# Kernel tuning notes

Measured on AMD Instinct MI355X. Metric: run time of the kernel, lower is better.

The kernel has to match this reference:

```python
import jax, jax.numpy as jnp
import numpy as np

# Gate hyperparameters (from init_kwargs)
DIM = 4096
N_EXPERTS = 256        # n_routed_experts
N_GROUPS = 8           # n_expert_groups
TOPK_GROUPS = 4        # n_limited_groups
TOPK = 8               # n_activated_experts
ROUTE_SCALE = 1.0
N_TOKENS = 16384       # batch * seq_len flattened


def setup_inputs() -> dict:
    key = jax.random.key(0)
    kx, kw = jax.random.split(key)
    x = jax.random.normal(kx, (N_TOKENS, DIM), dtype=jnp.float32)
    # xavier-ish scale for the gate projection weight [n_experts, dim]
    weight = jax.random.normal(kw, (N_EXPERTS, DIM), dtype=jnp.float32) * (1.0 / np.sqrt(DIM))
    return {"x": x, "weight": weight}


def reference(x, weight):
    T = x.shape[0]
    # scores = linear(x, weight)  -> [T, E]
    logits = jnp.einsum('td,ed->te', x, weight)
    # score_func == 'softmax' computed in fp32 (torch: softmax(dim=-1, dtype=float32))
    scores = jax.nn.softmax(logits.astype(jnp.float32), axis=-1)
    original_scores = scores

    # group-limited routing (n_groups > 1, no bias -> amax per group)
    sg = scores.reshape(T, N_GROUPS, N_EXPERTS // N_GROUPS)   # [T, G, E/G]
    group_scores = jnp.max(sg, axis=-1)                        # [T, G]
    _, gidx = jax.lax.top_k(group_scores, TOPK_GROUPS)         # [T, topk_groups]
    keep = jnp.zeros((T, N_GROUPS), dtype=bool)
    keep = keep.at[jnp.arange(T)[:, None], gidx].set(True)
    masked = jnp.where(keep[:, :, None], sg, -jnp.inf).reshape(T, N_EXPERTS)

    # top-k expert selection; weights gathered from the un-masked scores
    _, idx = jax.lax.top_k(masked, TOPK)                       # [T, topk]
    weights = jnp.take_along_axis(original_scores, idx, axis=1)
    weights = weights * ROUTE_SCALE
    return weights.astype(x.dtype), idx
```

## Files before the change

### kernel.cpp

```cpp
#include <hip/hip_runtime.h>
#include <math.h>
#include <stdint.h>

#define NTOK   16384
#define DIM    4096
#define NEXP   256
#define TOPKG  4
#define TOPK   8
#define NSPLIT 4
#define KCHUNK (DIM / NSPLIT)
#define BM     256
#define BK     32
#define NSTEPS (KCHUNK / BK)

typedef float v4f   __attribute__((ext_vector_type(4)));
typedef short short8 __attribute__((ext_vector_type(8)));

__device__ inline unsigned short f2bf(float x) {
    unsigned u = __float_as_uint(x);
    return (unsigned short)((u + 0x7fffu + ((u >> 16) & 1u)) >> 16);
}
__device__ inline float bf2f(unsigned short h) {
    return __uint_as_float(((unsigned)h) << 16);
}
__device__ inline int swz4(int row, int slot) { return slot ^ ((row >> 1) & 3); }

__global__ __launch_bounds__(256) void wprep(const float* __restrict__ W,
                                             unsigned short* __restrict__ Wh,
                                             unsigned short* __restrict__ Wl) {
    int i = (blockIdx.x * 256 + threadIdx.x) * 4;
    float4 v = *(const float4*)(W + i);
    ushort4 h, l;
    h.x = f2bf(v.x); l.x = f2bf(v.x - bf2f(h.x));
    h.y = f2bf(v.y); l.y = f2bf(v.y - bf2f(h.y));
    h.z = f2bf(v.z); l.z = f2bf(v.z - bf2f(h.z));
    h.w = f2bf(v.w); l.w = f2bf(v.w - bf2f(h.w));
    *(ushort4*)(Wh + i) = h;
    *(ushort4*)(Wl + i) = l;
}

__global__ __launch_bounds__(512, 2) void gate_gemm(const float* __restrict__ X,
                                                    const unsigned short* __restrict__ Wh,
                                                    const unsigned short* __restrict__ Wl,
                                                    float* __restrict__ P) {
    __shared__ __align__(16) unsigned short Ah[2][BM * BK];
    __shared__ __align__(16) unsigned short Al[2][BM * BK];
    __shared__ __align__(16) unsigned short Bh[2][NEXP * BK];
    __shared__ __align__(16) unsigned short Bl[2][NEXP * BK];

    const int t  = threadIdx.x;
    const int bm = blockIdx.x * BM;
    const int z  = blockIdx.y;
    const int k0 = z * KCHUNK;

    const int l  = t & 63;
    const int w  = t >> 6;
    const int wr = w >> 2;
    const int wc = w & 3;
    const int lm = l & 15;
    const int lq = l >> 4;

    const int ar = t >> 1;
    const float* xrow = X + (size_t)(bm + ar) * DIM + k0 + (t & 1) * 16;

    v4f acc[8][4] = {};

    {
#pragma unroll
        for (int i = 0; i < 2; ++i) {
            int flat = i * 512 + t;
            int e = flat >> 2, qq = flat & 3;
            const unsigned short* gh = Wh + (size_t)e * DIM + k0 + swz4(e, qq) * 8;
            const unsigned short* gl = Wl + (size_t)e * DIM + k0 + swz4(e, qq) * 8;
            __builtin_amdgcn_global_load_lds(
                (const __attribute__((address_space(1))) unsigned int*)gh,
                (__attribute__((address_space(3))) unsigned int*)&Bh[0][flat * 8], 16, 0, 0);
            __builtin_amdgcn_global_load_lds(
                (const __attribute__((address_space(1))) unsigned int*)gl,
                (__attribute__((address_space(3))) unsigned int*)&Bl[0][flat * 8], 16, 0, 0);
        }
        float4 xv0[4];
#pragma unroll
        for (int i = 0; i < 4; ++i) xv0[i] = *(const float4*)(xrow + i * 4);
#pragma unroll
        for (int i = 0; i < 4; ++i) {
            ushort4 h, lo;
            h.x = f2bf(xv0[i].x); lo.x = f2bf(xv0[i].x - bf2f(h.x));
            h.y = f2bf(xv0[i].y); lo.y = f2bf(xv0[i].y - bf2f(h.y));
            h.z = f2bf(xv0[i].z); lo.z = f2bf(xv0[i].z - bf2f(h.z));
            h.w = f2bf(xv0[i].w); lo.w = f2bf(xv0[i].w - bf2f(h.w));
            int j = (t & 1) * 4 + i;
            int idx = ar * BK + swz4(ar, j >> 1) * 8 + (j & 1) * 4;
            *(ushort4*)&Ah[0][idx] = h;
            *(ushort4*)&Al[0][idx] = lo;
        }
        __syncthreads();
    }

    int cur = 0;
    for (int s = 0; s < NSTEPS; ++s) {
        const int nxt = cur ^ 1;
        const bool pf = (s + 1 < NSTEPS);
        const int krn = (pf ? s + 1 : s) * BK;

        short8 bh[4], bl[4];
        float4 xv[4];

#pragma unroll
        for (int q = 0; q < 4; ++q) {
            if (q == 0) {
#pragma unroll
                for (int c = 0; c < 4; ++c) {
                    int e = wc * 64 + c * 16 + lm;
                    bh[c] = *(const short8*)&Bh[cur][e * BK + swz4(e, lq) * 8];
                    bl[c] = *(const short8*)&Bl[cur][e * BK + swz4(e, lq) * 8];
                }
            }
            const int m0 = wr * 128 + (2 * q) * 16 + lm;
            const int m1 = m0 + 16;
            short8 a0h = *(const short8*)&Ah[cur][m0 * BK + swz4(m0, lq) * 8];
            short8 a0l = *(const short8*)&Al[cur][m0 * BK + swz4(m0, lq) * 8];
            short8 a1h = *(const short8*)&Ah[cur][m1 * BK + swz4(m1, lq) * 8];
            short8 a1l = *(const short8*)&Al[cur][m1 * BK + swz4(m1, lq) * 8];

            if (pf) {
                if (q == 0) {
#pragma unroll
                    for (int i = 0; i < 4; ++i) xv[i] = *(const float4*)(xrow + krn + i * 4);
#pragma unroll
                    for (int i = 0; i < 2; ++i) {
                        int flat = i * 512 + t;
                        int e = flat >> 2, qq = flat & 3;
                        const unsigned short* g = Wh + (size_t)e * DIM + k0 + krn + swz4(e, qq) * 8;
                        __builtin_amdgcn_global_load_lds(
                            (const __attribute__((address_space(1))) unsigned int*)g,
                            (__attribute__((address_space(3))) unsigned int*)&Bh[nxt][flat * 8], 16, 0, 0);
                    }
                } else if (q == 1) {
#pragma unroll
                    for (int i = 0; i < 2; ++i) {
                        int flat = i * 512 + t;
                        int e = flat >> 2, qq = flat & 3;
                        const unsigned short* g = Wl + (size_t)e * DIM + k0 + krn + swz4(e, qq) * 8;
                        __builtin_amdgcn_global_load_lds(
                            (const __attribute__((address_space(1))) unsigned int*)g,
                            (__attribute__((address_space(3))) unsigned int*)&Bl[nxt][flat * 8], 16, 0, 0);
                    }
                } else {
                    const int i0 = (q == 2) ? 0 : 2;
#pragma unroll
                    for (int i = i0; i < i0 + 2; ++i) {
                        ushort4 h, lo;
                        h.x = f2bf(xv[i].x); lo.x = f2bf(xv[i].x - bf2f(h.x));
                        h.y = f2bf(xv[i].y); lo.y = f2bf(xv[i].y - bf2f(h.y));
                        h.z = f2bf(xv[i].z); lo.z = f2bf(xv[i].z - bf2f(h.z));
                        h.w = f2bf(xv[i].w); lo.w = f2bf(xv[i].w - bf2f(h.w));
                        int j = (t & 1) * 4 + i;
                        int idx = ar * BK + swz4(ar, j >> 1) * 8 + (j & 1) * 4;
                        *(ushort4*)&Ah[nxt][idx] = h;
                        *(ushort4*)&Al[nxt][idx] = lo;
                    }
                }
            }

            if (q == 0) asm volatile("s_waitcnt lgkmcnt(8)");
            __builtin_amdgcn_s_barrier();
            asm volatile("s_waitcnt lgkmcnt(0)");
            __builtin_amdgcn_sched_barrier(0);
            __builtin_amdgcn_s_setprio(1);
#pragma unroll
            for (int c = 0; c < 4; ++c) {
                acc[2 * q][c] = __builtin_amdgcn_mfma_f32_16x16x32_bf16(a0h, bh[c], acc[2 * q][c], 0, 0, 0);
                acc[2 * q][c] = __builtin_amdgcn_mfma_f32_16x16x32_bf16(a0h, bl[c], acc[2 * q][c], 0, 0, 0);
                acc[2 * q][c] = __builtin_amdgcn_mfma_f32_16x16x32_bf16(a0l, bh[c], acc[2 * q][c], 0, 0, 0);
            }
#pragma unroll
            for (int c = 0; c < 4; ++c) {
                acc[2 * q + 1][c] = __builtin_amdgcn_mfma_f32_16x16x32_bf16(a1h, bh[c], acc[2 * q + 1][c], 0, 0, 0);
                acc[2 * q + 1][c] = __builtin_amdgcn_mfma_f32_16x16x32_bf16(a1h, bl[c], acc[2 * q + 1][c], 0, 0, 0);
                acc[2 * q + 1][c] = __builtin_amdgcn_mfma_f32_16x16x32_bf16(a1l, bh[c], acc[2 * q + 1][c], 0, 0, 0);
            }
            __builtin_amdgcn_s_setprio(0);
            if (q < 3) __builtin_amdgcn_s_barrier();
            else       __syncthreads();
        }
        cur = nxt;
    }

    float* Pb = P + ((size_t)z * NTOK + bm) * NEXP;
#pragma unroll
    for (int r = 0; r < 8; ++r)
#pragma unroll
        for (int c = 0; c < 4; ++c)
#pragma unroll
            for (int g = 0; g < 4; ++g)
                Pb[(size_t)(wr * 128 + r * 16 + lq * 4 + g) * NEXP + wc * 64 + c * 16 + lm] = acc[r][c][g];
}

__global__ __launch_bounds__(256) void gate_route(const float* __restrict__ P,
                                                  float* __restrict__ outw,
                                                  float* __restrict__ outi) {
    const int lane = threadIdx.x & 63;
    const int tok  = (blockIdx.x * blockDim.x + threadIdx.x) >> 6;
    if (tok >= NTOK) return;

    float l[4] = {0.f, 0.f, 0.f, 0.f};
#pragma unroll
    for (int z = 0; z < NSPLIT; ++z) {
        float4 v = *(const float4*)(P + ((size_t)z * NTOK + tok) * NEXP + lane * 4);
        l[0] += v.x; l[1] += v.y; l[2] += v.z; l[3] += v.w;
    }

    float lmax = fmaxf(fmaxf(l[0], l[1]), fmaxf(l[2], l[3]));
    float m = lmax;
#pragma unroll
    for (int o = 32; o; o >>= 1) m = fmaxf(m, __shfl_xor(m, o));

    float s = __expf(l[0] - m) + __expf(l[1] - m) + __expf(l[2] - m) + __expf(l[3] - m);
#pragma unroll
    for (int o = 32; o; o >>= 1) s += __shfl_xor(s, o);

    float gm = lmax;
#pragma unroll
    for (int o = 4; o; o >>= 1) gm = fmaxf(gm, __shfl_xor(gm, o));

    const int g = lane >> 3;
    int rank = 0;
#pragma unroll
    for (int gg = 0; gg < 8; ++gg) {
        float vg = __shfl(gm, gg * 8);
        rank += (vg > gm) || (vg == gm && gg < g);
    }
    const bool allowed = rank < TOPKG;

    float mv[4];
#pragma unroll
    for (int j = 0; j < 4; ++j) mv[j] = allowed ? l[j] : -INFINITY;

    float wsel = 0.0f;
    int   isel = 0;

    for (int k = 0; k < TOPK; ++k) {
        float bv = mv[0];
        int   bi = lane * 4;
        if (mv[1] > bv) { bv = mv[1]; bi = lane * 4 + 1; }
        if (mv[2] > bv) { bv = mv[2]; bi = lane * 4 + 2; }
        if (mv[3] > bv) { bv = mv[3]; bi = lane * 4 + 3; }
#pragma unroll
        for (int o = 32; o; o >>= 1) {
            float ov = __shfl_xor(bv, o);
            int   oi = __shfl_xor(bi, o);
            if (ov > bv || (ov == bv && oi < bi)) { bv = ov; bi = oi; }
        }
        if (lane == k) { wsel = __expf(bv - m) / s; isel = bi; }
        if ((bi >> 2) == lane) mv[bi & 3] = -INFINITY;
    }

    if (lane < TOPK) {
        outw[(size_t)tok * TOPK + lane] = wsel;
        outi[(size_t)tok * TOPK + lane] = (float)isel;
    }
}

extern "C" void kernel_launch(void* const* d_in, const int* in_sizes, int n_in,
                              void* d_out, int out_size, void* d_ws, size_t ws_size,
                              hipStream_t stream) {
    const float* x  = (const float*)d_in[0];
    const float* wt = (const float*)d_in[1];

    float* P = (float*)d_ws;
    unsigned short* Wh = (unsigned short*)((char*)d_ws + (size_t)NSPLIT * NTOK * NEXP * 4);
    unsigned short* Wl = Wh + (size_t)NEXP * DIM;

    float* outw = (float*)d_out;
    float* outi = (float*)d_out + (size_t)NTOK * TOPK;

    wprep<<<(NEXP * DIM) / (256 * 4), 256, 0, stream>>>(wt, Wh, Wl);

    dim3 ggrid(NTOK / BM, NSPLIT);
    gate_gemm<<<ggrid, 512, 0, stream>>>(x, Wh, Wl, P);

    gate_route<<<(NTOK * 64) / 256, 256, 0, stream>>>(P, outw, outi);
}
```

Measured before the change: 438.6 us.

## Prepack weight hi/lo tiles contiguously and simplify GEMM pipeline to one barrier per step

The weight prep kernel now writes the bf16 hi/lo split into a pre-swizzled, per-K-step contiguous layout, so each GEMM step copies one contiguous block into LDS. The inner loop drops the four-phase interleaved barrier schedule and uses a single prefetch, compute, convert, sync sequence per K step. The 1D grid is remapped so that blocks sharing a K-split are grouped together, and the partial-result stores become nontemporal. This cuts address math and barriers, but removes the fine-grained overlap of X conversion with MFMA work.

```diff
diff --git a/kernel.cpp b/kernel.cpp
--- a/kernel.cpp
+++ b/kernel.cpp
@@ -26,32 +26,39 @@
 __device__ inline int swz4(int row, int slot) { return slot ^ ((row >> 1) & 3); }
 
 __global__ __launch_bounds__(256) void wprep(const float* __restrict__ W,
-                                             unsigned short* __restrict__ Wh,
-                                             unsigned short* __restrict__ Wl) {
-    int i = (blockIdx.x * 256 + threadIdx.x) * 4;
-    float4 v = *(const float4*)(W + i);
-    ushort4 h, l;
-    h.x = f2bf(v.x); l.x = f2bf(v.x - bf2f(h.x));
-    h.y = f2bf(v.y); l.y = f2bf(v.y - bf2f(h.y));
-    h.z = f2bf(v.z); l.z = f2bf(v.z - bf2f(h.z));
-    h.w = f2bf(v.w); l.w = f2bf(v.w - bf2f(h.w));
-    *(ushort4*)(Wh + i) = h;
-    *(ushort4*)(Wl + i) = l;
+                                             unsigned short* __restrict__ Wp) {
+    int u  = blockIdx.x * 256 + threadIdx.x;
+    int zs = u >> 11;
+    int c  = u & 2047;
+    int z  = zs >> 5, s = zs & 31;
+    int half = c >> 10;
+    int cc = c & 1023;
+    int e  = cc >> 2, sl = cc & 3;
+    int sig = swz4(e, sl);
+    const float* src = W + (size_t)e * DIM + z * KCHUNK + s * BK + sig * 8;
+    float4 v0 = *(const float4*)src;
+    float4 v1 = *(const float4*)(src + 4);
+    float xf[8] = {v0.x, v0.y, v0.z, v0.w, v1.x, v1.y, v1.z, v1.w};
+    short8 out;
+#pragma unroll
+    for (int j = 0; j < 8; ++j) {
+        unsigned short h = f2bf(xf[j]);
+        out[j] = half ? (short)f2bf(xf[j] - bf2f(h)) : (short)h;
+    }
+    *(short8*)(Wp + (size_t)u * 8) = out;
 }
 
 __global__ __launch_bounds__(512, 2) void gate_gemm(const float* __restrict__ X,
-                                                    const unsigned short* __restrict__ Wh,
-                                                    const unsigned short* __restrict__ Wl,
+                                                    const unsigned short* __restrict__ Wp,
                                                     float* __restrict__ P) {
+    __shared__ __align__(16) unsigned short Bbuf[2][NEXP * BK * 2];
     __shared__ __align__(16) unsigned short Ah[2][BM * BK];
     __shared__ __align__(16) unsigned short Al[2][BM * BK];
-    __shared__ __align__(16) unsigned short Bh[2][NEXP * BK];
-    __shared__ __align__(16) unsigned short Bl[2][NEXP * BK];
-
-    const int t  = threadIdx.x;
-    const int bm = blockIdx.x * BM;
-    const int z  = blockIdx.y;
-    const int k0 = z * KCHUNK;
+
+    const int t = threadIdx.x;
+    const int b  = blockIdx.x;
+    const int z  = (b & 7) >> 1;
+    const int bm = (2 * (b >> 3) + (b & 1)) * BM;
 
     const int l  = t & 63;
     const int w  = t >> 6;
@@ -60,28 +67,24 @@
     const int lm = l & 15;
     const int lq = l >> 4;
 
+    const unsigned short* wz = Wp + (size_t)z * NSTEPS * (NEXP * BK * 2);
+
     const int ar = t >> 1;
-    const float* xrow = X + (size_t)(bm + ar) * DIM + k0 + (t & 1) * 16;
+    const float* xrow = X + (size_t)(bm + ar) * DIM + z * KCHUNK + (t & 1) * 16;
 
     v4f acc[8][4] = {};
 
     {
-#pragma unroll
-        for (int i = 0; i < 2; ++i) {
-            int flat = i * 512 + t;
-            int e = flat >> 2, qq = flat & 3;
-            const unsigned short* gh = Wh + (size_t)e * DIM + k0 + swz4(e, qq) * 8;
-            const unsigned short* gl = Wl + (size_t)e * DIM + k0 + swz4(e, qq) * 8;
+        float4 xv0[4];
+#pragma unroll
+        for (int i = 0; i < 4; ++i) xv0[i] = *(const float4*)(xrow + i * 4);
+#pragma unroll
+        for (int j = 0; j < 4; ++j) {
+            int flat = j * 512 + t;
             __builtin_amdgcn_global_load_lds(
-                (const __attribute__((address_space(1))) unsigned int*)gh,
-                (__attribute__((address_space(3))) unsigned int*)&Bh[0][flat * 8], 16, 0, 0);
-            __builtin_amdgcn_global_load_lds(
-                (const __attribute__((address_space(1))) unsigned int*)gl,
-                (__attribute__((address_space(3))) unsigned int*)&Bl[0][flat * 8], 16, 0, 0);
-        }
-        float4 xv0[4];
-#pragma unroll
-        for (int i = 0; i < 4; ++i) xv0[i] = *(const float4*)(xrow + i * 4);
+                (const __attribute__((address_space(1))) unsigned int*)(wz + flat * 8),
+                (__attribute__((address_space(3))) unsigned int*)&Bbuf[0][flat * 8], 16, 0, 0);
+        }
 #pragma unroll
         for (int i = 0; i < 4; ++i) {
             ushort4 h, lo;
@@ -101,89 +104,61 @@
     for (int s = 0; s < NSTEPS; ++s) {
         const int nxt = cur ^ 1;
         const bool pf = (s + 1 < NSTEPS);
-        const int krn = (pf ? s + 1 : s) * BK;
+
+        float4 xv[4];
+        if (pf) {
+#pragma unroll
+            for (int i = 0; i < 4; ++i) xv[i] = *(const float4*)(xrow + (s + 1) * BK + i * 4);
+            const unsigned short* wsrc = wz + (size_t)(s + 1) * (NEXP * BK * 2);
+#pragma unroll
+            for (int j = 0; j < 4; ++j) {
+                int flat = j * 512 + t;
+                __builtin_amdgcn_global_load_lds(
+                    (const __attribute__((address_space(1))) unsigned int*)(wsrc + flat * 8),
+                    (__attribute__((address_space(3))) unsigned int*)&Bbuf[nxt][flat * 8], 16, 0, 0);
+            }
+        }
+        __builtin_amdgcn_sched_barrier(0);
 
         short8 bh[4], bl[4];
-        float4 xv[4];
-
-#pragma unroll
-        for (int q = 0; q < 4; ++q) {
-            if (q == 0) {
-#pragma unroll
-                for (int c = 0; c < 4; ++c) {
-                    int e = wc * 64 + c * 16 + lm;
-                    bh[c] = *(const short8*)&Bh[cur][e * BK + swz4(e, lq) * 8];
-                    bl[c] = *(const short8*)&Bl[cur][e * BK + swz4(e, lq) * 8];
-                }
+#pragma unroll
+        for (int c = 0; c < 4; ++c) {
+            int e = wc * 64 + c * 16 + lm;
+            bh[c] = *(const short8*)&Bbuf[cur][e * BK + swz4(e, lq) * 8];
+            bl[c] = *(const short8*)&Bbuf[cur][NEXP * BK + e * BK + swz4(e, lq) * 8];
+        }
+        __builtin_amdgcn_s_setprio(1);
+#pragma unroll
+        for (int r = 0; r < 8; ++r) {
+            int m = wr * 128 + r * 16 + lm;
+            short8 ah = *(const short8*)&Ah[cur][m * BK + swz4(m, lq) * 8];
+            short8 al = *(const short8*)&Al[cur][m * BK + swz4(m, lq) * 8];
+#pragma unroll
+            for (int c = 0; c < 4; ++c) {
+                acc[r][c] = __builtin_amdgcn_mfma_f32_16x16x32_bf16(ah, bh[c], acc[r][c], 0, 0, 0);
+                acc[r][c] = __builtin_amdgcn_mfma_f32_16x16x32_bf16(ah, bl[c], acc[r][c], 0, 0, 0);
+                acc[r][c] = __builtin_amdgcn_mfma_f32_16x16x32_bf16(al, bh[c], acc[r][c], 0, 0, 0);
             }
-            const int m0 = wr * 128 + (2 * q) * 16 + lm;
-            const int m1 = m0 + 16;
-            short8 a0h = *(const short8*)&Ah[cur][m0 * BK + swz4(m0, lq) * 8];
-            short8 a0l = *(const short8*)&Al[cur][m0 * BK + swz4(m0, lq) * 8];
-            short8 a1h = *(const short8*)&Ah[cur][m1 * BK + swz4(m1, lq) * 8];
-            short8 a1l = *(const short8*)&Al[cur][m1 * BK + swz4(m1, lq) * 8];
-
-            if (pf) {
-                if (q == 0) {
-#pragma unroll
-                    for (int i = 0; i < 4; ++i) xv[i] = *(const float4*)(xrow + krn + i * 4);
-#pragma unroll
-                    for (int i = 0; i < 2; ++i) {
-                        int flat = i * 512 + t;
-                        int e = flat >> 2, qq = flat & 3;
-                        const unsigned short* g = Wh + (size_t)e * DIM + k0 + krn + swz4(e, qq) * 8;
-                        __builtin_amdgcn_global_load_lds(
-                            (const __attribute__((address_space(1))) unsigned int*)g,
-                            (__attribute__((address_space(3))) unsigned int*)&Bh[nxt][flat * 8], 16, 0, 0);
-                    }
-                } else if (q == 1) {
-#pragma unroll
-                    for (int i = 0; i < 2; ++i) {
-                        int flat = i * 512 + t;
-                        int e = flat >> 2, qq = flat & 3;
-                        const unsigned short* g = Wl + (size_t)e * DIM + k0 + krn + swz4(e, qq) * 8;
-                        __builtin_amdgcn_global_load_lds(
-                            (const __attribute__((address_space(1))) unsigned int*)g,
-                            (__attribute__((address_space(3))) unsigned int*)&Bl[nxt][flat * 8], 16, 0, 0);
-                    }
-                } else {
-                    const int i0 = (q == 2) ? 0 : 2;
-#pragma unroll
-                    for (int i = i0; i < i0 + 2; ++i) {
-                        ushort4 h, lo;
-                        h.x = f2bf(xv[i].x); lo.x = f2bf(xv[i].x - bf2f(h.x));
-                        h.y = f2bf(xv[i].y); lo.y = f2bf(xv[i].y - bf2f(h.y));
-                        h.z = f2bf(xv[i].z); lo.z = f2bf(xv[i].z - bf2f(h.z));
-                        h.w = f2bf(xv[i].w); lo.w = f2bf(xv[i].w - bf2f(h.w));
-                        int j = (t & 1) * 4 + i;
-                        int idx = ar * BK + swz4(ar, j >> 1) * 8 + (j & 1) * 4;
-                        *(ushort4*)&Ah[nxt][idx] = h;
-                        *(ushort4*)&Al[nxt][idx] = lo;
-                    }
-                }
+        }
+        __builtin_amdgcn_s_setprio(0);
+        __builtin_amdgcn_sched_barrier(0);
+
+        if (pf) {
+#pragma unroll
+            for (int i = 0; i < 4; ++i) {
+                ushort4 h, lo;
+                h.x = f2bf(xv[i].x); lo.x = f2bf(xv[i].x - bf2f(h.x));
+                h.y = f2bf(xv[i].y); lo.y = f2bf(xv[i].y - bf2f(h.y));
+                h.z = f2bf(xv[i].z); lo.z = f2bf(xv[i].z - bf2f(h.z));
+                h.w = f2bf(xv[i].w); lo.w = f2bf(xv[i].w - bf2f(h.w));
+                int j = (t & 1) * 4 + i;
+                int idx = ar * BK + swz4(ar, j >> 1) * 8 + (j & 1) * 4;
+                *(ushort4*)&Ah[nxt][idx] = h;
+                *(ushort4*)&Al[nxt][idx] = lo;
             }
-
-            if (q == 0) asm volatile("s_waitcnt lgkmcnt(8)");
-            __builtin_amdgcn_s_barrier();
-            asm volatile("s_waitcnt lgkmcnt(0)");
-            __builtin_amdgcn_sched_barrier(0);
-            __builtin_amdgcn_s_setprio(1);
-#pragma unroll
-            for (int c = 0; c < 4; ++c) {
-                acc[2 * q][c] = __builtin_amdgcn_mfma_f32_16x16x32_bf16(a0h, bh[c], acc[2 * q][c], 0, 0, 0);
-                acc[2 * q][c] = __builtin_amdgcn_mfma_f32_16x16x32_bf16(a0h, bl[c], acc[2 * q][c], 0, 0, 0);
-                acc[2 * q][c] = __builtin_amdgcn_mfma_f32_16x16x32_bf16(a0l, bh[c], acc[2 * q][c], 0, 0, 0);
-            }
-#pragma unroll
-            for (int c = 0; c < 4; ++c) {
-                acc[2 * q + 1][c] = __builtin_amdgcn_mfma_f32_16x16x32_bf16(a1h, bh[c], acc[2 * q + 1][c], 0, 0, 0);
-                acc[2 * q + 1][c] = __builtin_amdgcn_mfma_f32_16x16x32_bf16(a1h, bl[c], acc[2 * q + 1][c], 0, 0, 0);
-                acc[2 * q + 1][c] = __builtin_amdgcn_mfma_f32_16x16x32_bf16(a1l, bh[c], acc[2 * q + 1][c], 0, 0, 0);
-            }
-            __builtin_amdgcn_s_setprio(0);
-            if (q < 3) __builtin_amdgcn_s_barrier();
-            else       __syncthreads();
-        }
+        }
+
+        __syncthreads();
         cur = nxt;
     }
 
@@ -194,7 +169,8 @@
         for (int c = 0; c < 4; ++c)
 #pragma unroll
             for (int g = 0; g < 4; ++g)
-                Pb[(size_t)(wr * 128 + r * 16 + lq * 4 + g) * NEXP + wc * 64 + c * 16 + lm] = acc[r][c][g];
+                __builtin_nontemporal_store(acc[r][c][g],
+                    &Pb[(size_t)(wr * 128 + r * 16 + lq * 4 + g) * NEXP + wc * 64 + c * 16 + lm]);
 }
 
 __global__ __launch_bounds__(256) void gate_route(const float* __restrict__ P,
@@ -269,16 +245,14 @@
     const float* wt = (const float*)d_in[1];
 
     float* P = (float*)d_ws;
-    unsigned short* Wh = (unsigned short*)((char*)d_ws + (size_t)NSPLIT * NTOK * NEXP * 4);
-    unsigned short* Wl = Wh + (size_t)NEXP * DIM;
+    unsigned short* Wp = (unsigned short*)((char*)d_ws + (size_t)NSPLIT * NTOK * NEXP * 4);
 
     float* outw = (float*)d_out;
     float* outi = (float*)d_out + (size_t)NTOK * TOPK;
 
-    wprep<<<(NEXP * DIM) / (256 * 4), 256, 0, stream>>>(wt, Wh, Wl);
-
-    dim3 ggrid(NTOK / BM, NSPLIT);
-    gate_gemm<<<ggrid, 512, 0, stream>>>(x, Wh, Wl, P);
+    wprep<<<1024, 256, 0, stream>>>(wt, Wp);
+
+    gate_gemm<<<256, 512, 0, stream>>>(x, Wp, P);
 
     gate_route<<<(NTOK * 64) / 256, 256, 0, stream>>>(P, outw, outi);
 }
```

Result: slower. 475.7 us (+8.5%).

## Deepen GEMM prefetch pipeline with explicit vmcnt waits and two-step-ahead X loads

Applied to the files above, without the earlier changes.

Restructures the split-K gate GEMM main loop. X rows are now loaded into registers two K-steps ahead. Both hi and lo weight stages are issued together at the first sub-step via global_load_lds. The bf16 hi/lo conversion of X happens at sub-step 2, guarded by explicit s_waitcnt vmcnt counts instead of full __syncthreads. This is meant to hide global-load latency behind MFMA work and cut synchronization overhead, at the cost of hand-counted memory waits that depend on in-order vmcnt completion and on slightly higher register pressure.

```diff
diff --git a/kernel.cpp b/kernel.cpp
--- a/kernel.cpp
+++ b/kernel.cpp
@@ -63,49 +63,69 @@
     const int ar = t >> 1;
     const float* xrow = X + (size_t)(bm + ar) * DIM + k0 + (t & 1) * 16;
 
+#define BSTAGE(buf, step)                                                           \
+    do {                                                                            \
+        const int krn_ = (step) * BK;                                               \
+        _Pragma("unroll")                                                           \
+        for (int i_ = 0; i_ < 2; ++i_) {                                            \
+            int flat_ = i_ * 512 + t;                                               \
+            int e_ = flat_ >> 2, qq_ = flat_ & 3;                                   \
+            const unsigned short* gh_ = Wh + (size_t)e_ * DIM + k0 + krn_ + swz4(e_, qq_) * 8; \
+            const unsigned short* gl_ = Wl + (size_t)e_ * DIM + k0 + krn_ + swz4(e_, qq_) * 8; \
+            __builtin_amdgcn_global_load_lds(                                       \
+                (const __attribute__((address_space(1))) unsigned int*)gh_,         \
+                (__attribute__((address_space(3))) unsigned int*)&Bh[buf][flat_ * 8], 16, 0, 0); \
+            __builtin_amdgcn_global_load_lds(                                       \
+                (const __attribute__((address_space(1))) unsigned int*)gl_,         \
+                (__attribute__((address_space(3))) unsigned int*)&Bl[buf][flat_ * 8], 16, 0, 0); \
+        }                                                                           \
+    } while (0)
+
+#define ACONV(buf, v0, v1, v2, v3)                                                  \
+    do {                                                                            \
+        float4 xa_[4] = {v0, v1, v2, v3};                                           \
+        _Pragma("unroll")                                                           \
+        for (int i_ = 0; i_ < 4; ++i_) {                                            \
+            ushort4 h_, lo_;                                                        \
+            h_.x = f2bf(xa_[i_].x); lo_.x = f2bf(xa_[i_].x - bf2f(h_.x));           \
+            h_.y = f2bf(xa_[i_].y); lo_.y = f2bf(xa_[i_].y - bf2f(h_.y));           \
+            h_.z = f2bf(xa_[i_].z); lo_.z = f2bf(xa_[i_].z - bf2f(h_.z));           \
+            h_.w = f2bf(xa_[i_].w); lo_.w = f2bf(xa_[i_].w - bf2f(h_.w));           \
+            int j_ = (t & 1) * 4 + i_;                                              \
+            int idx_ = ar * BK + swz4(ar, j_ >> 1) * 8 + (j_ & 1) * 4;              \
+            *(ushort4*)&Ah[buf][idx_] = h_;                                         \
+            *(ushort4*)&Al[buf][idx_] = lo_;                                        \
+        }                                                                           \
+    } while (0)
+
     v4f acc[8][4] = {};
+    float4 xv0, xv1, xv2, xv3;
 
     {
-#pragma unroll
-        for (int i = 0; i < 2; ++i) {
-            int flat = i * 512 + t;
-            int e = flat >> 2, qq = flat & 3;
-            const unsigned short* gh = Wh + (size_t)e * DIM + k0 + swz4(e, qq) * 8;
-            const unsigned short* gl = Wl + (size_t)e * DIM + k0 + swz4(e, qq) * 8;
-            __builtin_amdgcn_global_load_lds(
-                (const __attribute__((address_space(1))) unsigned int*)gh,
-                (__attribute__((address_space(3))) unsigned int*)&Bh[0][flat * 8], 16, 0, 0);
-            __builtin_amdgcn_global_load_lds(
-                (const __attribute__((address_space(1))) unsigned int*)gl,
-                (__attribute__((address_space(3))) unsigned int*)&Bl[0][flat * 8], 16, 0, 0);
-        }
-        float4 xv0[4];
-#pragma unroll
-        for (int i = 0; i < 4; ++i) xv0[i] = *(const float4*)(xrow + i * 4);
-#pragma unroll
-        for (int i = 0; i < 4; ++i) {
-            ushort4 h, lo;
-            h.x = f2bf(xv0[i].x); lo.x = f2bf(xv0[i].x - bf2f(h.x));
-            h.y = f2bf(xv0[i].y); lo.y = f2bf(xv0[i].y - bf2f(h.y));
-            h.z = f2bf(xv0[i].z); lo.z = f2bf(xv0[i].z - bf2f(h.z));
-            h.w = f2bf(xv0[i].w); lo.w = f2bf(xv0[i].w - bf2f(h.w));
-            int j = (t & 1) * 4 + i;
-            int idx = ar * BK + swz4(ar, j >> 1) * 8 + (j & 1) * 4;
-            *(ushort4*)&Ah[0][idx] = h;
-            *(ushort4*)&Al[0][idx] = lo;
-        }
-        __syncthreads();
+        float4 p0 = *(const float4*)(xrow);
+        float4 p1 = *(const float4*)(xrow + 4);
+        float4 p2 = *(const float4*)(xrow + 8);
+        float4 p3 = *(const float4*)(xrow + 12);
+        BSTAGE(0, 0);
+        asm volatile("s_waitcnt vmcnt(4)" ::: "memory");
+        __builtin_amdgcn_sched_barrier(0);
+        ACONV(0, p0, p1, p2, p3);
+        xv0 = *(const float4*)(xrow + BK);
+        xv1 = *(const float4*)(xrow + BK + 4);
+        xv2 = *(const float4*)(xrow + BK + 8);
+        xv3 = *(const float4*)(xrow + BK + 12);
+        asm volatile("s_waitcnt vmcnt(4)" ::: "memory");
+        asm volatile("s_waitcnt lgkmcnt(0)" ::: "memory");
+        __builtin_amdgcn_sched_barrier(0);
+        __builtin_amdgcn_s_barrier();
     }
 
     int cur = 0;
     for (int s = 0; s < NSTEPS; ++s) {
         const int nxt = cur ^ 1;
         const bool pf = (s + 1 < NSTEPS);
-        const int krn = (pf ? s + 1 : s) * BK;
 
         short8 bh[4], bl[4];
-        float4 xv[4];
-
 #pragma unroll
         for (int q = 0; q < 4; ++q) {
             if (q == 0) {
@@ -123,49 +143,31 @@
             short8 a1h = *(const short8*)&Ah[cur][m1 * BK + swz4(m1, lq) * 8];
             short8 a1l = *(const short8*)&Al[cur][m1 * BK + swz4(m1, lq) * 8];
 
-            if (pf) {
-                if (q == 0) {
-#pragma unroll
-                    for (int i = 0; i < 4; ++i) xv[i] = *(const float4*)(xrow + krn + i * 4);
-#pragma unroll
-                    for (int i = 0; i < 2; ++i) {
-                        int flat = i * 512 + t;
-                        int e = flat >> 2, qq = flat & 3;
-                        const unsigned short* g = Wh + (size_t)e * DIM + k0 + krn + swz4(e, qq) * 8;
-                        __builtin_amdgcn_global_load_lds(
-                            (const __attribute__((address_space(1))) unsigned int*)g,
-                            (__attribute__((address_space(3))) unsigned int*)&Bh[nxt][flat * 8], 16, 0, 0);
-                    }
-                } else if (q == 1) {
-#pragma unroll
-                    for (int i = 0; i < 2; ++i) {
-                        int flat = i * 512 + t;
-                        int e = flat >> 2, qq = flat & 3;
-                        const unsigned short* g = Wl + (size_t)e * DIM + k0 + krn + swz4(e, qq) * 8;
-                        __builtin_amdgcn_global_load_lds(
-                            (const __attribute__((address_space(1))) unsigned int*)g,
-                            (__attribute__((address_space(3))) unsigned int*)&Bl[nxt][flat * 8], 16, 0, 0);
-                    }
-                } else {
-                    const int i0 = (q == 2) ? 0 : 2;
-#pragma unroll
-                    for (int i = i0; i < i0 + 2; ++i) {
-                        ushort4 h, lo;
-                        h.x = f2bf(xv[i].x); lo.x = f2bf(xv[i].x - bf2f(h.x));
-                        h.y = f2bf(xv[i].y); lo.y = f2bf(xv[i].y - bf2f(h.y));
-                        h.z = f2bf(xv[i].z); lo.z = f2bf(xv[i].z - bf2f(h.z));
-                        h.w = f2bf(xv[i].w); lo.w = f2bf(xv[i].w - bf2f(h.w));
-                        int j = (t & 1) * 4 + i;
-                        int idx = ar * BK + swz4(ar, j >> 1) * 8 + (j & 1) * 4;
-                        *(ushort4*)&Ah[nxt][idx] = h;
-                        *(ushort4*)&Al[nxt][idx] = lo;
-                    }
+            if (q == 0 && pf) {
+                BSTAGE(nxt, s + 1);
+            }
+            if (q == 2 && pf) {
+                asm volatile("s_waitcnt vmcnt(4)" ::: "memory");
+                __builtin_amdgcn_sched_barrier(0);
+                ACONV(nxt, xv0, xv1, xv2, xv3);
+            }
+            if (q == 3) {
+                if (s + 2 < NSTEPS) {
+                    const float* xn = xrow + (s + 2) * BK;
+                    xv0 = *(const float4*)(xn);
+                    xv1 = *(const float4*)(xn + 4);
+                    xv2 = *(const float4*)(xn + 8);
+                    xv3 = *(const float4*)(xn + 12);
+                    asm volatile("s_waitcnt vmcnt(4)" ::: "memory");
+                    __builtin_amdgcn_sched_barrier(0);
+                } else if (pf) {
+                    asm volatile("s_waitcnt vmcnt(0)" ::: "memory");
+                    __builtin_amdgcn_sched_barrier(0);
                 }
             }
 
-            if (q == 0) asm volatile("s_waitcnt lgkmcnt(8)");
             __builtin_amdgcn_s_barrier();
-            asm volatile("s_waitcnt lgkmcnt(0)");
+            asm volatile("s_waitcnt lgkmcnt(0)" ::: "memory");
             __builtin_amdgcn_sched_barrier(0);
             __builtin_amdgcn_s_setprio(1);
 #pragma unroll
@@ -181,8 +183,7 @@
                 acc[2 * q + 1][c] = __builtin_amdgcn_mfma_f32_16x16x32_bf16(a1l, bh[c], acc[2 * q + 1][c], 0, 0, 0);
             }
             __builtin_amdgcn_s_setprio(0);
-            if (q < 3) __builtin_amdgcn_s_barrier();
-            else       __syncthreads();
+            __builtin_amdgcn_s_barrier();
         }
         cur = nxt;
     }
@@ -195,6 +196,8 @@
 #pragma unroll
             for (int g = 0; g < 4; ++g)
                 Pb[(size_t)(wr * 128 + r * 16 + lq * 4 + g) * NEXP + wc * 64 + c * 16 + lm] = acc[r][c][g];
+#undef BSTAGE
+#undef ACONV
 }
 
 __global__ __launch_bounds__(256) void gate_route(const float* __restrict__ P,
```

Result: faster. 429.8 us (-2.0%).
